# Kernel optimization log

Measured on AMD Instinct MI355X. Metric: run time of the kernel, lower is better.

Reference implementation:

```python
import jax, jax.numpy as jnp
import numpy as np

B, D_IN, H, HV, A, E, HW = 16384, 512, 512, 256, 32, 8, 512

def _lin(key, fan_in, fan_out):
    k1, k2 = jax.random.split(key)
    s = 1.0 / np.sqrt(fan_in)
    W = jax.random.uniform(k1, (fan_in, fan_out), minval=-s, maxval=s, dtype=jnp.float32)
    b = jax.random.uniform(k2, (fan_out,), minval=-s, maxval=s, dtype=jnp.float32)
    return W, b

def _stack(key, n, fan_in, fan_out):
    Ws, bs = [], []
    for k in jax.random.split(key, n):
        W, b = _lin(k, fan_in, fan_out)
        Ws.append(W); bs.append(b)
    return jnp.stack(Ws), jnp.stack(bs)

def setup_inputs() -> dict:
    key = jax.random.key(0)
    ks = jax.random.split(key, 16)
    x = jax.random.normal(ks[0], (B, D_IN), dtype=jnp.float32)
    # stacked expert policy nets: in->H, H->H, H->A (tanh)
    Wp0, bp0 = _stack(ks[1], E, D_IN, H)
    Wp1, bp1 = _stack(ks[2], E, H, H)
    Wmu, bmu = _stack(ks[3], E, H, A)
    # stacked expert value nets (hardcoded 256 hidden in source): in->256, 256->256, 256->1
    Wv0, bv0 = _stack(ks[4], E, D_IN, HV)
    Wv1, bv1 = _stack(ks[5], E, HV, HV)
    Wv, bv = _stack(ks[6], E, HV, 1)
    # gating net: in->HW, HW->HW, HW->E, softmax
    Ww0, bw0 = _lin(ks[7], D_IN, HW)
    Ww1, bw1 = _lin(ks[8], HW, HW)
    Wwo, bwo = _lin(ks[9], HW, E)
    return dict(x=x, Wp0=Wp0, bp0=bp0, Wp1=Wp1, bp1=bp1, Wmu=Wmu, bmu=bmu,
                Wv0=Wv0, bv0=bv0, Wv1=Wv1, bv1=bv1, Wv=Wv, bv=bv,
                Ww0=Ww0, bw0=bw0, Ww1=Ww1, bw1=bw1, Wwo=Wwo, bwo=bwo)

def reference(x, Wp0, bp0, Wp1, bp1, Wmu, bmu, Wv0, bv0, Wv1, bv1, Wv, bv,
              Ww0, bw0, Ww1, bw1, Wwo, bwo):
    # experts as one grouped/batched GEMM over axis e
    h = jax.nn.relu(jnp.einsum('bi,eih->ebh', x, Wp0) + bp0[:, None, :])      # [E,B,H]
    h = jax.nn.relu(jnp.einsum('ebh,ehk->ebk', h, Wp1) + bp1[:, None, :])
    actions = jnp.tanh(jnp.einsum('ebh,eha->eba', h, Wmu) + bmu[:, None, :])  # [E,B,A]
    # per-expert values
    g = jax.nn.relu(jnp.einsum('bi,eih->ebh', x, Wv0) + bv0[:, None, :])      # [E,B,HV]
    g = jax.nn.relu(jnp.einsum('ebh,ehk->ebk', g, Wv1) + bv1[:, None, :])
    values = jnp.einsum('ebh,eho->ebo', g, Wv) + bv[:, None, :]               # [E,B,1]
    # gating network + softmax
    u = jax.nn.relu(x @ Ww0 + bw0)
    u = jax.nn.relu(u @ Ww1 + bw1)
    w = jax.nn.softmax(u @ Wwo + bwo, axis=-1)                                # [B,E]
    # Categorical(w).sample() with a fixed key, then per-row gather of values
    pis = jax.random.categorical(jax.random.key(42), jnp.log(w), axis=-1)     # [B] int
    v = values[pis, jnp.arange(values.shape[1])]                              # [B,1]
    return actions, v, w
```

## Files before the change

kernel.cpp:

```cpp
#include <hip/hip_runtime.h>


typedef float   f32x4 __attribute__((ext_vector_type(4)));
typedef _Float16 f16;
typedef _Float16 f16x4 __attribute__((ext_vector_type(4)));
typedef _Float16 f16x8 __attribute__((ext_vector_type(8)));

typedef __attribute__((address_space(1))) unsigned int gas_u32;
typedef __attribute__((address_space(3))) unsigned int las_u32;

__device__ __forceinline__ void gl_lds16(const void* g, void* l) {
  __builtin_amdgcn_global_load_lds((gas_u32*)g, (las_u32*)l, 16, 0, 0);
}

__device__ __forceinline__ int xcd_swz(int b, int G) {
  int q = G >> 3, r = G & 7;
  int x = b & 7, y = b >> 3;
  return (x < r ? x * (q + 1) : r * (q + 1) + (x - r) * q) + y;
}

template<int EPI>
__global__ __launch_bounds__(512, 4) void gemm3_kernel(
    const f16* __restrict__ A, const f16* __restrict__ BT,
    const float* __restrict__ bias, void* __restrict__ Cv,
    const int K, const int lda, const int ldc,
    const long long sAe, const long long sCe,
    const int mT, const int nInner, const int eShift)
{
  constexpr int BM = 256, BN = 128;
  __shared__ __align__(16) char sm[(BM + BN) * 128];
  char* Ash = sm;
  char* Bsh = sm + BM * 128;

  const int tid = threadIdx.x;
  const int lane = tid & 63;
  const int wid = tid >> 6;
  const int wr = wid >> 1, wc = wid & 1;

  const int L = xcd_swz(blockIdx.x, gridDim.x);
  const int nIn = L % nInner;
  const int m = (L / nInner) % mT;
  const int eo = L / (nInner * mT);
  const int nv0 = (eo * nInner + nIn) * BN;
  const int e = nv0 >> eShift;
  const int col0 = nv0 & ((1 << eShift) - 1);
  const int m0 = m * BM;

  const f16* Ab = A + (size_t)sAe * e + (size_t)m0 * lda;
  const f16* Bb = BT + (size_t)nv0 * K;

  f32x4 acc[4][4] = {};
  const int ksteps = K >> 6;

  for (int kt = 0; kt < ksteps; ++kt) {
    __syncthreads();
    const f16* Ak = Ab + (kt << 6);
    const f16* Bk = Bb + (kt << 6);
    #pragma unroll
    for (int u0 = 0; u0 < BM * 8; u0 += 512) {
      int u = u0 + tid;
      int row = u >> 3;
      int kb = ((u & 7) << 4) ^ ((row & 7) << 4);
      gl_lds16(Ak + (size_t)row * lda + (kb >> 1), Ash + u * 16);
    }
    #pragma unroll
    for (int u0 = 0; u0 < BN * 8; u0 += 512) {
      int u = u0 + tid;
      int row = u >> 3;
      int kb = ((u & 7) << 4) ^ ((row & 7) << 4);
      gl_lds16(Bk + (size_t)row * K + (kb >> 1), Bsh + u * 16);
    }
    __syncthreads();

    f16x8 af[4][2], bf[4][2];
    const int kl = (lane >> 4) << 4;
    #pragma unroll
    for (int fm = 0; fm < 4; ++fm) {
      int row = wr * 64 + fm * 16 + (lane & 15);
      int sw = (row & 7) << 4;
      af[fm][0] = *(const f16x8*)(Ash + row * 128 + (kl ^ sw));
      af[fm][1] = *(const f16x8*)(Ash + row * 128 + ((64 + kl) ^ sw));
    }
    #pragma unroll
    for (int fn = 0; fn < 4; ++fn) {
      int row = wc * 64 + fn * 16 + (lane & 15);
      int sw = (row & 7) << 4;
      bf[fn][0] = *(const f16x8*)(Bsh + row * 128 + (kl ^ sw));
      bf[fn][1] = *(const f16x8*)(Bsh + row * 128 + ((64 + kl) ^ sw));
    }
    #pragma unroll
    for (int fm = 0; fm < 4; ++fm)
      #pragma unroll
      for (int fn = 0; fn < 4; ++fn) {
        acc[fm][fn] = __builtin_amdgcn_mfma_f32_16x16x32_f16(
            bf[fn][0], af[fm][0], acc[fm][fn], 0, 0, 0);
        acc[fm][fn] = __builtin_amdgcn_mfma_f32_16x16x32_f16(
            bf[fn][1], af[fm][1], acc[fm][fn], 0, 0, 0);
      }
  }

  const int rbase = m0 + wr * 64 + (lane & 15);
  const int cb = wc * 64 + ((lane >> 4) << 2);
  #pragma unroll
  for (int fm = 0; fm < 4; ++fm) {
    const int row = rbase + fm * 16;
    #pragma unroll
    for (int fn = 0; fn < 4; ++fn) {
      const int bcol = cb + fn * 16;
      const int col = col0 + bcol;
      f32x4 v = acc[fm][fn];
      f32x4 bb = *(const f32x4*)(bias + nv0 + bcol);
      if constexpr (EPI == 0) {
        f16x4 h;
        #pragma unroll
        for (int r = 0; r < 4; ++r) h[r] = (f16)fmaxf(v[r] + bb[r], 0.0f);
        *(f16x4*)((f16*)Cv + (size_t)sCe * e + (size_t)row * ldc + col) = h;
      } else if constexpr (EPI == 2) {
        f32x4 o;
        #pragma unroll
        for (int r = 0; r < 4; ++r) o[r] = fmaxf(v[r] + bb[r], 0.0f);
        *(f32x4*)((float*)Cv + (size_t)sCe * e + (size_t)row * ldc + col) = o;
      } else {
        f16x4 h, l, s;
        #pragma unroll
        for (int r = 0; r < 4; ++r) {
          float u = fmaxf(v[r] + bb[r], 0.0f);
          f16 hh = (f16)u;
          float hv = (float)hh;
          h[r] = hh;
          l[r] = (f16)((u - hv) * 32.0f);
          s[r] = (f16)(hv * 0.03125f);
        }
        f16* cp = (f16*)Cv + (size_t)sCe * e + (size_t)row * ldc + col;
        *(f16x4*)(cp) = h;
        *(f16x4*)(cp + 512) = l;
        *(f16x4*)(cp + 1024) = s;
      }
    }
  }
}

template<int BM, int BN, int WM, int WN, int EPI>
__global__ __launch_bounds__(256, 2) void gemm2_kernel(
    const f16* __restrict__ A, const f16* __restrict__ BT,
    const float* __restrict__ bias, void* __restrict__ Cv,
    const int K, const int lda, const int ldc,
    const long long sAe, const long long sCe,
    const int mT, const int nInner, const int eShift)
{
  constexpr int FM = WM / 16, FN = WN / 16;
  constexpr int WAVES_N = BN / WN;
  __shared__ __align__(16) char sm[(BM + BN) * 128];
  char* Ash = sm;
  char* Bsh = sm + BM * 128;

  const int tid = threadIdx.x;
  const int lane = tid & 63;
  const int wid = tid >> 6;

  const int L = xcd_swz(blockIdx.x, gridDim.x);
  const int nIn = L % nInner;
  const int m = (L / nInner) % mT;
  const int eo = L / (nInner * mT);
  const int nv0 = (eo * nInner + nIn) * BN;
  const int e = nv0 >> eShift;
  const int col0 = nv0 & ((1 << eShift) - 1);
  const int m0 = m * BM;

  const f16* Ab = A + (size_t)sAe * e + (size_t)m0 * lda;
  const f16* Bb = BT + (size_t)nv0 * K;
  const int wr = wid / WAVES_N, wc = wid % WAVES_N;

  f32x4 acc[FM][FN] = {};
  const int ksteps = K >> 6;

  for (int kt = 0; kt < ksteps; ++kt) {
    __syncthreads();
    const f16* Ak = Ab + (kt << 6);
    const f16* Bk = Bb + (kt << 6);
    for (int u0 = 0; u0 < BM * 8; u0 += 256) {
      int u = u0 + tid;
      int row = u >> 3;
      int kb = ((u & 7) << 4) ^ ((row & 7) << 4);
      gl_lds16(Ak + (size_t)row * lda + (kb >> 1), Ash + u * 16);
    }
    for (int u0 = 0; u0 < BN * 8; u0 += 256) {
      int u = u0 + tid;
      int row = u >> 3;
      int kb = ((u & 7) << 4) ^ ((row & 7) << 4);
      gl_lds16(Bk + (size_t)row * K + (kb >> 1), Bsh + u * 16);
    }
    __syncthreads();

    f16x8 af[FM][2], bf[FN][2];
    const int kl = (lane >> 4) << 4;
    #pragma unroll
    for (int fm = 0; fm < FM; ++fm) {
      int row = wr * WM + fm * 16 + (lane & 15);
      int sw = (row & 7) << 4;
      af[fm][0] = *(const f16x8*)(Ash + row * 128 + (kl ^ sw));
      af[fm][1] = *(const f16x8*)(Ash + row * 128 + ((64 + kl) ^ sw));
    }
    #pragma unroll
    for (int fn = 0; fn < FN; ++fn) {
      int row = wc * WN + fn * 16 + (lane & 15);
      int sw = (row & 7) << 4;
      bf[fn][0] = *(const f16x8*)(Bsh + row * 128 + (kl ^ sw));
      bf[fn][1] = *(const f16x8*)(Bsh + row * 128 + ((64 + kl) ^ sw));
    }
    #pragma unroll
    for (int fm = 0; fm < FM; ++fm)
      #pragma unroll
      for (int fn = 0; fn < FN; ++fn) {
        acc[fm][fn] = __builtin_amdgcn_mfma_f32_16x16x32_f16(
            bf[fn][0], af[fm][0], acc[fm][fn], 0, 0, 0);
        acc[fm][fn] = __builtin_amdgcn_mfma_f32_16x16x32_f16(
            bf[fn][1], af[fm][1], acc[fm][fn], 0, 0, 0);
      }
  }

  const int rbase = m0 + wr * WM + (lane & 15);
  const int cb = wc * WN + ((lane >> 4) << 2);
  #pragma unroll
  for (int fm = 0; fm < FM; ++fm) {
    const int row = rbase + fm * 16;
    #pragma unroll
    for (int fn = 0; fn < FN; ++fn) {
      const int bcol = cb + fn * 16;
      const int col = col0 + bcol;
      f32x4 v = acc[fm][fn];
      f32x4 bb = *(const f32x4*)(bias + nv0 + bcol);
      if constexpr (EPI == 0) {
        f16x4 h;
        #pragma unroll
        for (int r = 0; r < 4; ++r) h[r] = (f16)fmaxf(v[r] + bb[r], 0.0f);
        *(f16x4*)((f16*)Cv + (size_t)sCe * e + (size_t)row * ldc + col) = h;
      } else {
        f32x4 o;
        #pragma unroll
        for (int r = 0; r < 4; ++r) o[r] = tanhf(v[r] + bb[r]);
        *(f32x4*)((float*)Cv + (size_t)sCe * e + (size_t)row * ldc + col) = o;
      }
    }
  }
}

__global__ __launch_bounds__(256) void prep_kernel(
    const float* __restrict__ x, f16* __restrict__ xsplit,
    const float* __restrict__ Wp0, f16* __restrict__ Wp0T,
    const float* __restrict__ Wp1, f16* __restrict__ Wp1T,
    const float* __restrict__ Wmu, f16* __restrict__ WmuT,
    const float* __restrict__ Wv0, f16* __restrict__ Wv0T,
    const float* __restrict__ Wv1, f16* __restrict__ Wv1T,
    const float* __restrict__ Ww0, f16* __restrict__ Ww0T3,
    const float* __restrict__ Ww1, f16* __restrict__ Ww1T3)
{
  __shared__ float t[32][33];
  const int tid = threadIdx.x;
  int b = blockIdx.x;
  if (b < 8192) {
    const size_t i = ((size_t)b * 256 + tid) * 4;
    const int row = (int)(i >> 9);
    const int col = (int)(i & 511);
    f32x4 v = *(const f32x4*)(x + i);
    f16x4 h, l, s;
    #pragma unroll
    for (int j = 0; j < 4; ++j) {
      f16 hh = (f16)v[j];
      float hv = (float)hh;
      h[j] = hh;
      l[j] = (f16)((v[j] - hv) * 32.0f);
      s[j] = (f16)(hv * 0.03125f);
    }
    f16* p = xsplit + (size_t)row * 1536 + col;
    *(f16x4*)(p) = h;
    *(f16x4*)(p + 512) = l;
    *(f16x4*)(p + 1024) = s;
    return;
  }
  b -= 8192;
  const float* W;
  f16* T;
  bool triple = false;
  int K, N;
  if (b < 2048)               { W = Wp0; T = Wp0T; K = 512; N = 512; }
  else if ((b -= 2048) < 2048){ W = Wp1; T = Wp1T; K = 512; N = 512; }
  else if ((b -= 2048) < 128) { W = Wmu; T = WmuT; K = 512; N = 32; }
  else if ((b -= 128) < 1024) { W = Wv0; T = Wv0T; K = 512; N = 256; }
  else if ((b -= 1024) < 512) { W = Wv1; T = Wv1T; K = 256; N = 256; }
  else if ((b -= 512) < 256)  { W = Ww0; T = Ww0T3; triple = true; K = 512; N = 512; }
  else { b -= 256;              W = Ww1; T = Ww1T3; triple = true; K = 512; N = 512; }

  const int kT = K >> 5, nT = N >> 5;
  const int e = b / (kT * nT);
  const int rem = b % (kT * nT);
  const int k0 = (rem % kT) << 5;
  const int n0 = (rem / kT) << 5;
  const int tx = tid & 31, ty = tid >> 5;
  const float* Wp = W + (size_t)e * K * N;
  #pragma unroll
  for (int i = 0; i < 4; ++i)
    t[ty + i * 8][tx] = Wp[(size_t)(k0 + ty + i * 8) * N + n0 + tx];
  __syncthreads();
  #pragma unroll
  for (int i = 0; i < 4; ++i) {
    const int n = n0 + ty + i * 8, k = k0 + tx;
    float v = t[tx][ty + i * 8];
    f16 hh = (f16)v;
    if (!triple) {
      T[(size_t)e * K * N + (size_t)n * K + k] = hh;
    } else {
      float hv = (float)hh;
      f16* p = T + (size_t)n * 1536 + k;
      p[0] = hh;
      p[512] = (f16)(hv * 0.03125f);
      p[1024] = (f16)((v - hv) * 32.0f);
    }
  }
}

__global__ __launch_bounds__(256) void values_kernel(
    const f16* __restrict__ G2, const float* __restrict__ Wv,
    const float* __restrict__ bv, float* __restrict__ values, const int e0)
{
  const int tid = threadIdx.x, lane = tid & 63, wid = tid >> 6;
  const int gi = blockIdx.x * 4 + wid;
  const int el = gi >> 14;
  const int b = gi & 16383;
  const int eg = e0 + el;
  const f16* g = G2 + (((size_t)el << 14) + b) * 256 + (lane << 2);
  f16x4 gv = *(const f16x4*)g;
  const float* wv = Wv + ((size_t)eg << 8) + (lane << 2);
  float a = (float)gv[0] * wv[0] + (float)gv[1] * wv[1] +
            (float)gv[2] * wv[2] + (float)gv[3] * wv[3];
  #pragma unroll
  for (int off = 32; off >= 1; off >>= 1) a += __shfl_xor(a, off);
  if (lane == 0) values[((size_t)eg << 14) + b] = a + bv[eg];
}

__device__ __forceinline__ void threefry_0_42(unsigned x0, unsigned x1,
                                              unsigned& o0, unsigned& o1)
{
  const unsigned ks0 = 0u, ks1 = 42u, ks2 = 0x1BD11BDAu ^ 42u;
  x0 += ks0; x1 += ks1;
#define TF_R(r) { x0 += x1; x1 = (x1 << r) | (x1 >> (32 - r)); x1 ^= x0; }
  TF_R(13) TF_R(15) TF_R(26) TF_R(6)  x0 += ks1; x1 += ks2 + 1u;
  TF_R(17) TF_R(29) TF_R(16) TF_R(24) x0 += ks2; x1 += ks0 + 2u;
  TF_R(13) TF_R(15) TF_R(26) TF_R(6)  x0 += ks0; x1 += ks1 + 3u;
  TF_R(17) TF_R(29) TF_R(16) TF_R(24) x0 += ks1; x1 += ks2 + 4u;
  TF_R(13) TF_R(15) TF_R(26) TF_R(6)  x0 += ks2; x1 += ks0 + 5u;
#undef TF_R
  o0 = x0; o1 = x1;
}

__global__ __launch_bounds__(256) void gating_out_kernel(
    const float* __restrict__ U2, const float* __restrict__ Wwo,
    const float* __restrict__ bwo, const float* __restrict__ values,
    float* __restrict__ w_out, float* __restrict__ v_out)
{
  __shared__ float wl[4096];
  const int tid = threadIdx.x;
  for (int i = tid; i < 1024; i += 256)
    ((f32x4*)wl)[i] = ((const f32x4*)Wwo)[i];
  __syncthreads();
  const int lane = tid & 63, wid = tid >> 6;
  const int b = blockIdx.x * 4 + wid;

  const float* u = U2 + (size_t)b * 512 + lane * 8;
  f32x4 ua = *(const f32x4*)u;
  f32x4 ub = *(const f32x4*)(u + 4);
  float acc[8] = {};
  const float* wrow = wl + lane * 64;
  #pragma unroll
  for (int i = 0; i < 8; ++i) {
    float uv = (i < 4) ? ua[i] : ub[i - 4];
    #pragma unroll
    for (int ee = 0; ee < 8; ++ee) acc[ee] += uv * wrow[i * 8 + ee];
  }
  #pragma unroll
  for (int off = 32; off >= 1; off >>= 1)
    #pragma unroll
    for (int ee = 0; ee < 8; ++ee) acc[ee] += __shfl_xor(acc[ee], off);
  #pragma unroll
  for (int ee = 0; ee < 8; ++ee) acc[ee] += bwo[ee];

  float zmax = acc[0];
  #pragma unroll
  for (int ee = 1; ee < 8; ++ee) zmax = fmaxf(zmax, acc[ee]);
  float s = 0.0f;
  #pragma unroll
  for (int ee = 0; ee < 8; ++ee) s += expf(acc[ee] - zmax);

  float t0 = (lane & 1) ? acc[1] : acc[0];
  float t1 = (lane & 1) ? acc[3] : acc[2];
  float t2 = (lane & 1) ? acc[5] : acc[4];
  float t3 = (lane & 1) ? acc[7] : acc[6];
  float s0 = (lane & 2) ? t1 : t0;
  float s1 = (lane & 2) ? t3 : t2;
  float zown = (lane & 4) ? s1 : s0;

  if (lane < 8) w_out[(size_t)b * 8 + lane] = expf(zown - zmax) / s;

  unsigned idx = ((unsigned)b << 3) | (unsigned)(lane & 7);
  unsigned o0, o1;
  threefry_0_42(0u, idx, o0, o1);
  unsigned bits = o0 ^ o1;
  float f = __uint_as_float((bits >> 9) | 0x3F800000u) - 1.0f;
  f = fmaxf(f, 1.17549435e-38f);
  float g = -logf(-logf(f));
  float y = (lane < 8) ? (zown + g) : -3.0e38f;

  float best = __shfl(y, 0);
  int pi = 0;
  #pragma unroll
  for (int ee = 1; ee < 8; ++ee) {
    float ye = __shfl(y, ee);
    if (ye > best) { best = ye; pi = ee; }
  }
  if (lane == 0) v_out[b] = values[((size_t)pi << 14) + b];
}

extern "C" void kernel_launch(void* const* d_in, const int* in_sizes, int n_in,
                              void* d_out, int out_size, void* d_ws, size_t ws_size,
                              hipStream_t stream) {
  (void)in_sizes; (void)n_in; (void)out_size;
  const float* x   = (const float*)d_in[0];
  const float* Wp0 = (const float*)d_in[1];
  const float* bp0 = (const float*)d_in[2];
  const float* Wp1 = (const float*)d_in[3];
  const float* bp1 = (const float*)d_in[4];
  const float* Wmu = (const float*)d_in[5];
  const float* bmu = (const float*)d_in[6];
  const float* Wv0 = (const float*)d_in[7];
  const float* bv0 = (const float*)d_in[8];
  const float* Wv1 = (const float*)d_in[9];
  const float* bv1 = (const float*)d_in[10];
  const float* Wv  = (const float*)d_in[11];
  const float* bv  = (const float*)d_in[12];
  const float* Ww0 = (const float*)d_in[13];
  const float* bw0 = (const float*)d_in[14];
  const float* Ww1 = (const float*)d_in[15];
  const float* bw1 = (const float*)d_in[16];
  const float* Wwo = (const float*)d_in[17];
  const float* bwo = (const float*)d_in[18];

  float* out_actions = (float*)d_out;
  float* out_v = out_actions + (size_t)8 * 16384 * 32;
  float* out_w = out_v + 16384;

  char* base = (char*)d_ws;
  size_t off = 0;
  auto alloc = [&](size_t bytes) -> char* {
    char* p = base + off;
    off = (off + bytes + 255) & ~(size_t)255;
    return p;
  };

  f16* xsplit = (f16*)alloc((size_t)16384 * 1536 * 2);
  f16* Wp0T   = (f16*)alloc((size_t)8 * 512 * 512 * 2);
  f16* Wp1T   = (f16*)alloc((size_t)8 * 512 * 512 * 2);
  f16* WmuT   = (f16*)alloc((size_t)8 * 32 * 512 * 2);
  f16* Wv0T   = (f16*)alloc((size_t)8 * 256 * 512 * 2);
  f16* Wv1T   = (f16*)alloc((size_t)8 * 256 * 256 * 2);
  f16* Ww0T3  = (f16*)alloc((size_t)512 * 1536 * 2);
  f16* Ww1T3  = (f16*)alloc((size_t)512 * 1536 * 2);
  float* valuesBuf = (float*)alloc((size_t)8 * 16384 * 4);

  char* arena = base + off;
  const size_t avail = (ws_size > off) ? ws_size - off : 0;
  const size_t SZ67  = (size_t)67108864;
  const size_t SZ134 = (size_t)134217728;
  const bool full = avail >= SZ134 + SZ67;

  f16* P1 = (f16*)arena;
  f16* P2 = (f16*)(arena + (full ? SZ134 : SZ67));
  f16* VB1 = (f16*)arena;
  f16* VB2 = (f16*)(arena + SZ67);
  f16* U1split = (f16*)arena;
  float* U2 = (float*)(arena + (size_t)50331648);

  dim3 blk(256);
  dim3 blk8(512);
  const long long sBD = 16384LL * 512;
  const long long sBH = 16384LL * 256;

  prep_kernel<<<14464, blk, 0, stream>>>(
      x, xsplit, Wp0, Wp0T, Wp1, Wp1T, Wmu, WmuT, Wv0, Wv0T, Wv1, Wv1T,
      Ww0, Ww0T3, Ww1, Ww1T3);

  if (full) {
    gemm3_kernel<0><<<2048, blk8, 0, stream>>>(
        xsplit, Wp0T, bp0, P1, 512, 1536, 512, 0, sBD, 64, 32, 9);
    for (int e0 = 0; e0 < 8; e0 += 4) {
      gemm3_kernel<0><<<1024, blk8, 0, stream>>>(
          P1 + (size_t)e0 * sBD, Wp1T + (size_t)e0 * 512 * 512, bp1 + e0 * 512,
          P2, 512, 512, 512, sBD, sBD, 64, 4, 9);
      gemm2_kernel<128, 32, 32, 32, 1><<<512, blk, 0, stream>>>(
          P2, WmuT + (size_t)e0 * 32 * 512, bmu + e0 * 32,
          out_actions + (size_t)e0 * 16384 * 32,
          512, 512, 32, sBD, 16384LL * 32, 128, 1, 5);
    }
  } else {
    for (int e0 = 0; e0 < 8; e0 += 4) {
      gemm3_kernel<0><<<1024, blk8, 0, stream>>>(
          xsplit, Wp0T + (size_t)e0 * 512 * 512, bp0 + e0 * 512, P1,
          512, 1536, 512, 0, sBD, 64, 16, 9);
      gemm3_kernel<0><<<1024, blk8, 0, stream>>>(
          P1, Wp1T + (size_t)e0 * 512 * 512, bp1 + e0 * 512, P2,
          512, 512, 512, sBD, sBD, 64, 4, 9);
      gemm2_kernel<128, 32, 32, 32, 1><<<512, blk, 0, stream>>>(
          P2, WmuT + (size_t)e0 * 32 * 512, bmu + e0 * 32,
          out_actions + (size_t)e0 * 16384 * 32,
          512, 512, 32, sBD, 16384LL * 32, 128, 1, 5);
    }
  }

  gemm3_kernel<0><<<1024, blk8, 0, stream>>>(
      xsplit, Wv0T, bv0, VB1, 512, 1536, 256, 0, sBH, 64, 16, 8);
  gemm3_kernel<0><<<1024, blk8, 0, stream>>>(
      VB1, Wv1T, bv1, VB2, 256, 256, 256, sBH, sBH, 64, 2, 8);
  values_kernel<<<32768, blk, 0, stream>>>((const f16*)VB2, Wv, bv, valuesBuf, 0);

  gemm3_kernel<3><<<256, blk8, 0, stream>>>(
      xsplit, Ww0T3, bw0, U1split, 1536, 1536, 1536, 0, 0, 64, 4, 9);
  gemm3_kernel<2><<<256, blk8, 0, stream>>>(
      U1split, Ww1T3, bw1, U2, 1536, 1536, 512, 0, 0, 64, 4, 9);
  gating_out_kernel<<<4096, blk, 0, stream>>>(U2, Wwo, bwo, valuesBuf, out_w, out_v);
}
```

Measured before the change: 499.8 us.

## Add 256x256 ping-pong pipelined GEMM kernel for expert layers

Introduces a new GEMM kernel with 256x256 tiles, 512 threads, and a 128KB double-buffered LDS. It interleaves async global-to-LDS staging of the next tiles with quarter-tile MFMA bursts, separated by barriers, and raises MFMA wave priority. The expert policy and value GEMMs now use this kernel instead of the 256x128 gemm3 kernel, which should raise arithmetic intensity and overlap memory with compute. The path that ran all eight experts in one launch when the workspace was large enough is removed, so the policy path always runs in two halves. That adds launches, and with 128KB LDS only one block fits per CU, which limits occupancy.

Result: faster. 486.8 us (-2.6%).

```diff
diff --git a/kernel.cpp b/kernel.cpp
--- a/kernel.cpp
+++ b/kernel.cpp
@@ -17,6 +17,135 @@
   int q = G >> 3, r = G & 7;
   int x = b & 7, y = b >> 3;
   return (x < r ? x * (q + 1) : r * (q + 1) + (x - r) * q) + y;
+}
+
+__global__ __launch_bounds__(512, 2) void gemm8p_kernel(
+    const f16* __restrict__ A, const f16* __restrict__ BT,
+    const float* __restrict__ bias, f16* __restrict__ C,
+    const int K, const int lda, const int ldc,
+    const long long sAe, const long long sCe,
+    const int mT, const int nInner, const int eShift)
+{
+  __shared__ __align__(1024) char sm[131072];
+
+  const int tid = threadIdx.x;
+  const int lane = tid & 63;
+  const int wid = tid >> 6;
+  const int wr = wid >> 2, wc = wid & 3;
+  const int kl = (lane >> 4) << 4;
+  const int lm = lane & 15;
+
+  const int L = xcd_swz(blockIdx.x, gridDim.x);
+  const int nIn = L % nInner;
+  const int m = (L / nInner) % mT;
+  const int eo = L / (nInner * mT);
+  const int nv0 = (eo * nInner + nIn) << 8;
+  const int e = nv0 >> eShift;
+  const int col0 = nv0 & ((1 << eShift) - 1);
+  const int m0 = m << 8;
+
+  const f16* Ab = A + (size_t)sAe * e + (size_t)m0 * lda;
+  const f16* Bb = BT + (size_t)nv0 * K;
+  const int nt = K >> 6;
+
+  f32x4 acc[8][4] = {};
+  f16x8 af[4][2], bf0[2][2], bf1[2][2];
+
+#define STAGE_A(sp_, ta_, h_) { \
+  char* dst = sm + (((sp_) * 4 + (h_)) << 14); \
+  _Pragma("unroll") for (int i = 0; i < 2; ++i) { \
+    int u = tid + (i << 9); int p = u >> 3; \
+    const char* src = (const char*)(Ab + (size_t)(((p >> 6) << 7) + ((h_) << 6) + (p & 63)) * lda) \
+                      + ((size_t)(ta_) << 7) + (((u & 7) << 4) ^ ((p & 7) << 4)); \
+    gl_lds16(src, dst + u * 16); } }
+
+#define STAGE_B(sp_, ta_, h_) { \
+  char* dst = sm + (((sp_) * 4 + 2 + (h_)) << 14); \
+  _Pragma("unroll") for (int i = 0; i < 2; ++i) { \
+    int u = tid + (i << 9); int p = u >> 3; \
+    const char* src = (const char*)(Bb + (size_t)(((p >> 5) << 6) + ((h_) << 5) + (p & 31)) * K) \
+                      + ((size_t)(ta_) << 7) + (((u & 7) << 4) ^ ((p & 7) << 4)); \
+    gl_lds16(src, dst + u * 16); } }
+
+#define LDA(slot_) { _Pragma("unroll") for (int fm = 0; fm < 4; ++fm) { \
+    int p = (wr << 6) + (fm << 4) + lm; int sw = (p & 7) << 4; \
+    af[fm][0] = *(const f16x8*)((slot_) + p * 128 + (kl ^ sw)); \
+    af[fm][1] = *(const f16x8*)((slot_) + p * 128 + ((64 + kl) ^ sw)); } }
+
+#define LDB(bf_, slot_) { _Pragma("unroll") for (int fn = 0; fn < 2; ++fn) { \
+    int p = (wc << 5) + (fn << 4) + lm; int sw = (p & 7) << 4; \
+    bf_[fn][0] = *(const f16x8*)((slot_) + p * 128 + (kl ^ sw)); \
+    bf_[fn][1] = *(const f16x8*)((slot_) + p * 128 + ((64 + kl) ^ sw)); } }
+
+#define MFMA_Q(mh_, nh_, bf_) { \
+  __builtin_amdgcn_s_setprio(1); \
+  _Pragma("unroll") for (int fm = 0; fm < 4; ++fm) \
+  _Pragma("unroll") for (int fn = 0; fn < 2; ++fn) { \
+    acc[(mh_) * 4 + fm][(nh_) * 2 + fn] = __builtin_amdgcn_mfma_f32_16x16x32_f16( \
+        bf_[fn][0], af[fm][0], acc[(mh_) * 4 + fm][(nh_) * 2 + fn], 0, 0, 0); \
+    acc[(mh_) * 4 + fm][(nh_) * 2 + fn] = __builtin_amdgcn_mfma_f32_16x16x32_f16( \
+        bf_[fn][1], af[fm][1], acc[(mh_) * 4 + fm][(nh_) * 2 + fn], 0, 0, 0); } \
+  __builtin_amdgcn_s_setprio(0); }
+
+#define BAR __builtin_amdgcn_s_barrier()
+
+  STAGE_A(0, 0, 0); STAGE_B(0, 0, 0); STAGE_A(0, 0, 1); STAGE_B(0, 0, 1);
+  STAGE_A(1, 1, 0); STAGE_B(1, 1, 0);
+  asm volatile("s_waitcnt vmcnt(4)" ::: "memory");
+  __builtin_amdgcn_sched_barrier(0);
+  BAR;
+
+  for (int t = 0; t < nt; ++t) {
+    const int sp0 = t & 1, sp1 = sp0 ^ 1;
+    const int tp1 = (t + 1 < nt) ? t + 1 : t;
+    const int tp2 = (t + 2 < nt) ? t + 2 : t;
+    const char* sA0 = sm + ((sp0 * 4 + 0) << 14);
+    const char* sA1 = sm + ((sp0 * 4 + 1) << 14);
+    const char* sB0 = sm + ((sp0 * 4 + 2) << 14);
+    const char* sB1 = sm + ((sp0 * 4 + 3) << 14);
+
+    LDA(sA0); LDB(bf0, sB0);
+    STAGE_A(sp1, tp1, 1);
+    BAR; MFMA_Q(0, 0, bf0); BAR;
+
+    LDB(bf1, sB1);
+    STAGE_B(sp1, tp1, 1);
+    BAR; MFMA_Q(0, 1, bf1); BAR;
+
+    LDA(sA1);
+    STAGE_A(sp0, tp2, 0);
+    BAR; MFMA_Q(1, 0, bf0); BAR;
+
+    STAGE_B(sp0, tp2, 0);
+    asm volatile("s_waitcnt vmcnt(6)" ::: "memory");
+    __builtin_amdgcn_sched_barrier(0);
+    BAR; MFMA_Q(1, 1, bf1); BAR;
+  }
+  asm volatile("s_waitcnt vmcnt(0)" ::: "memory");
+
+#undef BAR
+#undef MFMA_Q
+#undef LDB
+#undef LDA
+#undef STAGE_B
+#undef STAGE_A
+
+  const int rbase = m0 + (wr << 7) + lm;
+  const int cb = (wc << 6) + ((lane >> 4) << 2);
+  #pragma unroll
+  for (int fa = 0; fa < 8; ++fa) {
+    const int row = rbase + fa * 16;
+    #pragma unroll
+    for (int fb = 0; fb < 4; ++fb) {
+      const int bcol = cb + fb * 16;
+      f32x4 v = acc[fa][fb];
+      f32x4 bb = *(const f32x4*)(bias + nv0 + bcol);
+      f16x4 h;
+      #pragma unroll
+      for (int r = 0; r < 4; ++r) h[r] = (f16)fmaxf(v[r] + bb[r], 0.0f);
+      *(f16x4*)(C + (size_t)sCe * e + (size_t)row * ldc + col0 + bcol) = h;
+    }
+  }
 }
 
 template<int EPI>
@@ -110,12 +239,7 @@
       const int col = col0 + bcol;
       f32x4 v = acc[fm][fn];
       f32x4 bb = *(const f32x4*)(bias + nv0 + bcol);
-      if constexpr (EPI == 0) {
-        f16x4 h;
-        #pragma unroll
-        for (int r = 0; r < 4; ++r) h[r] = (f16)fmaxf(v[r] + bb[r], 0.0f);
-        *(f16x4*)((f16*)Cv + (size_t)sCe * e + (size_t)row * ldc + col) = h;
-      } else if constexpr (EPI == 2) {
+      if constexpr (EPI == 2) {
         f32x4 o;
         #pragma unroll
         for (int r = 0; r < 4; ++r) o[r] = fmaxf(v[r] + bb[r], 0.0f);
@@ -140,7 +264,7 @@
   }
 }
 
-template<int BM, int BN, int WM, int WN, int EPI>
+template<int BM, int BN, int WM, int WN>
 __global__ __launch_bounds__(256, 2) void gemm2_kernel(
     const f16* __restrict__ A, const f16* __restrict__ BT,
     const float* __restrict__ bias, void* __restrict__ Cv,
@@ -230,17 +354,10 @@
       const int col = col0 + bcol;
       f32x4 v = acc[fm][fn];
       f32x4 bb = *(const f32x4*)(bias + nv0 + bcol);
-      if constexpr (EPI == 0) {
-        f16x4 h;
-        #pragma unroll
-        for (int r = 0; r < 4; ++r) h[r] = (f16)fmaxf(v[r] + bb[r], 0.0f);
-        *(f16x4*)((f16*)Cv + (size_t)sCe * e + (size_t)row * ldc + col) = h;
-      } else {
-        f32x4 o;
-        #pragma unroll
-        for (int r = 0; r < 4; ++r) o[r] = tanhf(v[r] + bb[r]);
-        *(f32x4*)((float*)Cv + (size_t)sCe * e + (size_t)row * ldc + col) = o;
-      }
+      f32x4 o;
+      #pragma unroll
+      for (int r = 0; r < 4; ++r) o[r] = tanhf(v[r] + bb[r]);
+      *(f32x4*)((float*)Cv + (size_t)sCe * e + (size_t)row * ldc + col) = o;
     }
   }
 }
@@ -423,7 +540,7 @@
 extern "C" void kernel_launch(void* const* d_in, const int* in_sizes, int n_in,
                               void* d_out, int out_size, void* d_ws, size_t ws_size,
                               hipStream_t stream) {
-  (void)in_sizes; (void)n_in; (void)out_size;
+  (void)in_sizes; (void)n_in; (void)out_size; (void)ws_size;
   const float* x   = (const float*)d_in[0];
   const float* Wp0 = (const float*)d_in[1];
   const float* bp0 = (const float*)d_in[2];
@@ -467,13 +584,9 @@
   float* valuesBuf = (float*)alloc((size_t)8 * 16384 * 4);
 
   char* arena = base + off;
-  const size_t avail = (ws_size > off) ? ws_size - off : 0;
-  const size_t SZ67  = (size_t)67108864;
-  const size_t SZ134 = (size_t)134217728;
-  const bool full = avail >= SZ134 + SZ67;
-
+  const size_t SZ67 = (size_t)67108864;
   f16* P1 = (f16*)arena;
-  f16* P2 = (f16*)(arena + (full ? SZ134 : SZ67));
+  f16* P2 = (f16*)(arena + SZ67);
   f16* VB1 = (f16*)arena;
   f16* VB2 = (f16*)(arena + SZ67);
   f16* U1split = (f16*)arena;
@@ -488,37 +601,23 @@
       x, xsplit, Wp0, Wp0T, Wp1, Wp1T, Wmu, WmuT, Wv0, Wv0T, Wv1, Wv1T,
       Ww0, Ww0T3, Ww1, Ww1T3);
 
-  if (full) {
-    gemm3_kernel<0><<<2048, blk8, 0, stream>>>(
-        xsplit, Wp0T, bp0, P1, 512, 1536, 512, 0, sBD, 64, 32, 9);
-    for (int e0 = 0; e0 < 8; e0 += 4) {
-      gemm3_kernel<0><<<1024, blk8, 0, stream>>>(
-          P1 + (size_t)e0 * sBD, Wp1T + (size_t)e0 * 512 * 512, bp1 + e0 * 512,
-          P2, 512, 512, 512, sBD, sBD, 64, 4, 9);
-      gemm2_kernel<128, 32, 32, 32, 1><<<512, blk, 0, stream>>>(
-          P2, WmuT + (size_t)e0 * 32 * 512, bmu + e0 * 32,
-          out_actions + (size_t)e0 * 16384 * 32,
-          512, 512, 32, sBD, 16384LL * 32, 128, 1, 5);
-    }
-  } else {
-    for (int e0 = 0; e0 < 8; e0 += 4) {
-      gemm3_kernel<0><<<1024, blk8, 0, stream>>>(
-          xsplit, Wp0T + (size_t)e0 * 512 * 512, bp0 + e0 * 512, P1,
-          512, 1536, 512, 0, sBD, 64, 16, 9);
-      gemm3_kernel<0><<<1024, blk8, 0, stream>>>(
-          P1, Wp1T + (size_t)e0 * 512 * 512, bp1 + e0 * 512, P2,
-          512, 512, 512, sBD, sBD, 64, 4, 9);
-      gemm2_kernel<128, 32, 32, 32, 1><<<512, blk, 0, stream>>>(
-          P2, WmuT + (size_t)e0 * 32 * 512, bmu + e0 * 32,
-          out_actions + (size_t)e0 * 16384 * 32,
-          512, 512, 32, sBD, 16384LL * 32, 128, 1, 5);
-    }
-  }
-
-  gemm3_kernel<0><<<1024, blk8, 0, stream>>>(
-      xsplit, Wv0T, bv0, VB1, 512, 1536, 256, 0, sBH, 64, 16, 8);
-  gemm3_kernel<0><<<1024, blk8, 0, stream>>>(
-      VB1, Wv1T, bv1, VB2, 256, 256, 256, sBH, sBH, 64, 2, 8);
+  for (int e0 = 0; e0 < 8; e0 += 4) {
+    gemm8p_kernel<<<512, blk8, 0, stream>>>(
+        xsplit, Wp0T + (size_t)e0 * 512 * 512, bp0 + e0 * 512, P1,
+        512, 1536, 512, 0, sBD, 64, 8, 9);
+    gemm8p_kernel<<<512, blk8, 0, stream>>>(
+        P1, Wp1T + (size_t)e0 * 512 * 512, bp1 + e0 * 512, P2,
+        512, 512, 512, sBD, sBD, 64, 2, 9);
+    gemm2_kernel<128, 32, 32, 32><<<512, blk, 0, stream>>>(
+        P2, WmuT + (size_t)e0 * 32 * 512, bmu + e0 * 32,
+        out_actions + (size_t)e0 * 16384 * 32,
+        512, 512, 32, sBD, 16384LL * 32, 128, 1, 5);
+  }
+
+  gemm8p_kernel<<<512, blk8, 0, stream>>>(
+      xsplit, Wv0T, bv0, VB1, 512, 1536, 256, 0, sBH, 64, 8, 8);
+  gemm8p_kernel<<<512, blk8, 0, stream>>>(
+      VB1, Wv1T, bv1, VB2, 256, 256, 256, sBH, sBH, 64, 1, 8);
   values_kernel<<<32768, blk, 0, stream>>>((const f16*)VB2, Wv, bv, valuesBuf, 0);
 
   gemm3_kernel<3><<<256, blk8, 0, stream>>>(
```
